# Performance work log

Measured on AMD Instinct MI355X. Metric: run time of the kernel, lower is better.

Reference implementation:

```python
import jax, jax.numpy as jnp
import numpy as np

NA = 100000
NB = 100000
N_REL = 6
REL_SRC = ['A', 'B', 'A', 'B', 'A', 'B']
REL_DST = ['B', 'A', 'A', 'B', 'B', 'A']
N_NODES = {'A': NA, 'B': NB}
H_DIM, OUT_DIM, N_BASES, N_EDGES = 64, 16, 4, 500000


def setup_inputs() -> dict:
    key = jax.random.key(0)
    ks = jax.random.split(key, 16)
    inp = {
        'embed_A': jax.random.normal(ks[0], (NA, H_DIM), jnp.float32) * 0.1,
        'embed_B': jax.random.normal(ks[1], (NB, H_DIM), jnp.float32) * 0.1,
        'bias0': jnp.zeros((H_DIM,), jnp.float32),
        'w_comp1': jax.random.normal(ks[2], (N_REL, N_BASES), jnp.float32) * 0.5,
        'basis1': jax.random.normal(ks[3], (N_BASES, H_DIM, H_DIM), jnp.float32) * (1.0 / np.sqrt(H_DIM)),
        'bias1': jnp.zeros((H_DIM,), jnp.float32),
        'w_comp2': jax.random.normal(ks[4], (N_REL, N_BASES), jnp.float32) * 0.5,
        'basis2': jax.random.normal(ks[5], (N_BASES, H_DIM, OUT_DIM), jnp.float32) * (1.0 / np.sqrt(H_DIM)),
        'bias2': jnp.zeros((OUT_DIM,), jnp.float32),
    }
    for r in range(N_REL):
        inp[f'src_r{r}'] = jax.random.randint(ks[6 + r], (N_EDGES,), 0, N_NODES[REL_SRC[r]], jnp.int32)
        inp[f'dst_r{r}'] = jax.random.randint(jax.random.fold_in(ks[6 + r], 7), (N_EDGES,), 0, N_NODES[REL_DST[r]], jnp.int32)
    return inp


def _hetero_conv(h, W_rels, bias, edges, out_dim, activation):
    # h: dict ntype -> [N, d_in]; W_rels: None or [n_rel, d_in, d_out]
    out = {nt: jnp.zeros((N_NODES[nt], out_dim), h['A'].dtype) for nt in N_NODES}
    for r in range(N_REL):
        src_t, dst_t = REL_SRC[r], REL_DST[r]
        src, dst = edges[r]
        x = h[src_t] if W_rels is None else h[src_t] @ W_rels[r]  # [N_src, d_out]
        msg = x[src]  # gather: [E, d_out]
        n_dst = N_NODES[dst_t]
        agg = jax.ops.segment_sum(msg, dst, num_segments=n_dst)
        deg = jax.ops.segment_sum(jnp.ones((msg.shape[0],), msg.dtype), dst, num_segments=n_dst)
        out[dst_t] = out[dst_t] + agg / jnp.maximum(deg, 1.0)[:, None]  # norm='right'
    out = {nt: out[nt] + bias for nt in out}
    if activation is not None:
        out = {nt: activation(out[nt]) for nt in out}
    return out


def reference(embed_A, embed_B, bias0, w_comp1, basis1, bias1, w_comp2, basis2, bias2,
              src_r0, dst_r0, src_r1, dst_r1, src_r2, dst_r2,
              src_r3, dst_r3, src_r4, dst_r4, src_r5, dst_r5):
    edges = [(src_r0, dst_r0), (src_r1, dst_r1), (src_r2, dst_r2),
             (src_r3, dst_r3), (src_r4, dst_r4), (src_r5, dst_r5)]
    h = {'A': embed_A, 'B': embed_B}
    # layer 0: weight=False -> pure normalized aggregation + bias + relu
    h = _hetero_conv(h, None, bias0, edges, H_DIM, jax.nn.relu)
    # hidden layer with basis-decomposed weights
    W1 = jnp.einsum('rb,bio->rio', w_comp1, basis1)
    h = _hetero_conv(h, W1, bias1, edges, H_DIM, jax.nn.relu)
    # output layer, no activation
    W2 = jnp.einsum('rb,bio->rio', w_comp2, basis2)
    h = _hetero_conv(h, W2, bias2, edges, OUT_DIM, None)
    return h['A']  # logits for category node type
```

## Files before the change

### kernel.cpp

```cpp
#include <hip/hip_runtime.h>

#define NN 100000
#define EE 500000
#define DD 64
#define OD 16
#define NR 6
#define NBASE 4
#define BSH 10
#define NBK 98
#define SBLK 128
#define FLATN (NBK * SBLK)
#define STCAP 5632

struct Edges { const int* src[NR]; const int* dst[NR]; };

typedef __attribute__((ext_vector_type(8))) short bf16x8;
typedef __attribute__((ext_vector_type(4))) float f32x4;

__device__ __forceinline__ float bf2f(ushort u) {
    union { unsigned int i; float f; } v; v.i = ((unsigned int)u) << 16; return v.f;
}
__device__ __forceinline__ ushort f2bf(float f) {
    unsigned int x = __float_as_uint(f);
    unsigned int r = (x + 0x7fffu + ((x >> 16) & 1u)) >> 16;
    return (ushort)r;
}
__device__ __forceinline__ void bfpair(unsigned int u, float& lo, float& hi) {
    lo = __uint_as_float(u << 16);
    hi = __uint_as_float(u & 0xffff0000u);
}

__global__ __launch_bounds__(256) void build_w_kernel(
    const float* __restrict__ wc1, const float* __restrict__ b1,
    const float* __restrict__ wc2, const float* __restrict__ b2,
    ushort* __restrict__ Wp1, ushort* __restrict__ Wp2)
{
    int idx = blockIdx.x * blockDim.x + threadIdx.x;
    const int n1 = NR * DD * DD;
    const int n2 = NR * DD * OD;
    if (idx < n1) {
        int r = idx >> 12, rem = idx & 4095;
        int i = rem >> 6, o = rem & 63;
        float s = 0.f;
        #pragma unroll
        for (int b = 0; b < NBASE; ++b) s += wc1[r * NBASE + b] * b1[b * 4096 + rem];
        Wp1[(((size_t)(r * 8 + (i >> 3)) * 64 + o) << 3) + (i & 7)] = f2bf(s);
    } else if (idx < n1 + n2) {
        int j = idx - n1;
        int r = j >> 10, rem = j & 1023;
        int i = rem >> 4, o = rem & 15;
        float s = 0.f;
        #pragma unroll
        for (int b = 0; b < NBASE; ++b) s += wc2[r * NBASE + b] * b2[b * 1024 + rem];
        Wp2[(((size_t)(r * 8 + (i >> 3)) * 16 + o) << 3) + (i & 7)] = f2bf(s);
    }
}

__global__ __launch_bounds__(256) void cvt_kernel(
    const float* __restrict__ in, ushort* __restrict__ out, int n4)
{
    int i = blockIdx.x * 256 + threadIdx.x;
    if (i >= n4) return;
    float4 v = ((const float4*)in)[i];
    ushort4 o;
    o.x = f2bf(v.x); o.y = f2bf(v.y); o.z = f2bf(v.z); o.w = f2bf(v.w);
    ((ushort4*)out)[i] = o;
}

__global__ __launch_bounds__(256) void count_kernel(Edges ep, int* __restrict__ cnt_mat)
{
    __shared__ int h[NBK];
    int r = blockIdx.y, blk = blockIdx.x;
    const int* __restrict__ dst = ep.dst[r];
    const int chunk = (EE + SBLK - 1) / SBLK;
    int e0 = blk * chunk, e1 = min(e0 + chunk, EE);
    for (int i = threadIdx.x; i < NBK; i += 256) h[i] = 0;
    __syncthreads();
    for (int e = e0 + threadIdx.x; e < e1; e += 256)
        atomicAdd(&h[dst[e] >> BSH], 1);
    __syncthreads();
    for (int b = threadIdx.x; b < NBK; b += 256)
        cnt_mat[r * FLATN + b * SBLK + blk] = h[b];
}

__global__ __launch_bounds__(1024) void flat_scan_kernel(
    const int* __restrict__ cnt_mat, int* __restrict__ off_flat, int* __restrict__ bbase)
{
    __shared__ int wsum[16];
    const int TPE = 13;
    int r = blockIdx.x;
    int tid = threadIdx.x, lane = tid & 63, wid = tid >> 6;
    int base = tid * TPE;
    int v[TPE];
    int s = 0;
    #pragma unroll
    for (int j = 0; j < TPE; ++j) {
        int i = base + j;
        v[j] = (i < FLATN) ? cnt_mat[r * FLATN + i] : 0;
        s += v[j];
    }
    int si = s;
    #pragma unroll
    for (int off = 1; off < 64; off <<= 1) {
        int t = __shfl_up(si, off);
        if (lane >= off) si += t;
    }
    if (lane == 63) wsum[wid] = si;
    __syncthreads();
    if (wid == 0) {
        int ws = (lane < 16) ? wsum[lane] : 0;
        #pragma unroll
        for (int off = 1; off < 16; off <<= 1) {
            int t = __shfl_up(ws, off);
            if (lane >= off) ws += t;
        }
        if (lane < 16) wsum[lane] = ws;
    }
    __syncthreads();
    int texcl = (wid > 0 ? wsum[wid - 1] : 0) + (si - s);
    int part = 0;
    #pragma unroll
    for (int j = 0; j < TPE; ++j) {
        int i = base + j;
        if (i < FLATN) {
            int o = texcl + part;
            off_flat[r * FLATN + i] = o;
            if ((i & (SBLK - 1)) == 0) bbase[r * (NBK + 1) + (i >> 7)] = o;
        }
        part += v[j];
    }
    if (tid == 0) bbase[r * (NBK + 1) + NBK] = EE;
}

__global__ __launch_bounds__(256) void scatter2_kernel(
    Edges ep, const int* __restrict__ off_flat, unsigned int* __restrict__ ebuf)
{
    __shared__ int goff[NBK];
    __shared__ int lcnt[NBK];
    int r = blockIdx.y, blk = blockIdx.x;
    const int* __restrict__ src = ep.src[r];
    const int* __restrict__ dst = ep.dst[r];
    unsigned int* eb = ebuf + (size_t)r * EE;
    const int chunk = (EE + SBLK - 1) / SBLK;
    int e0 = blk * chunk, e1 = min(e0 + chunk, EE);
    if (threadIdx.x < NBK) {
        goff[threadIdx.x] = off_flat[r * FLATN + threadIdx.x * SBLK + blk];
        lcnt[threadIdx.x] = 0;
    }
    __syncthreads();
    for (int e = e0 + threadIdx.x; e < e1; e += 256) {
        int d = dst[e];
        int b = d >> BSH;
        int pos = goff[b] + atomicAdd(&lcnt[b], 1);
        eb[pos] = (unsigned int)src[e] | ((unsigned int)(d & 1023) << 17);
    }
}

__global__ __launch_bounds__(256) void csr_fine_kernel(
    const unsigned int* __restrict__ ebuf, const int* __restrict__ bbase,
    int* __restrict__ row_ptr, float* __restrict__ inv_deg, int* __restrict__ col_idx)
{
    __shared__ int nh[1024];
    __shared__ int nb[1024];
    __shared__ int wsum4[4];
    __shared__ int stage[STCAP];
    int r = blockIdx.y, b = blockIdx.x;
    int tid = threadIdx.x, lane = tid & 63, wid = tid >> 6;
    int gb = bbase[r * (NBK + 1) + b];
    int ge = bbase[r * (NBK + 1) + b + 1];
    int cnt = ge - gb;
    if (cnt > STCAP) cnt = STCAP;
    const unsigned int* eb = ebuf + (size_t)r * EE + gb;
    #pragma unroll
    for (int j = 0; j < 4; ++j) nh[tid * 4 + j] = 0;
    __syncthreads();
    for (int i = tid; i < cnt; i += 256)
        atomicAdd(&nh[(eb[i] >> 17) & 1023], 1);
    __syncthreads();
    int v0 = nh[tid * 4 + 0], v1 = nh[tid * 4 + 1], v2 = nh[tid * 4 + 2], v3 = nh[tid * 4 + 3];
    int s = v0 + v1 + v2 + v3;
    int si = s;
    #pragma unroll
    for (int off = 1; off < 64; off <<= 1) {
        int t = __shfl_up(si, off);
        if (lane >= off) si += t;
    }
    if (lane == 63) wsum4[wid] = si;
    __syncthreads();
    if (tid == 0) {
        int a = 0;
        #pragma unroll
        for (int k = 0; k < 4; ++k) { int t = wsum4[k]; wsum4[k] = a; a += t; }
    }
    __syncthreads();
    int texcl = wsum4[wid] + (si - s);
    int p0 = texcl, p1 = p0 + v0, p2 = p1 + v1, p3 = p2 + v2;
    nb[tid * 4 + 0] = p0; nb[tid * 4 + 1] = p1; nb[tid * 4 + 2] = p2; nb[tid * 4 + 3] = p3;
    {
        int node0 = b * 1024 + tid * 4;
        int pj[4] = { p0, p1, p2, p3 };
        int vj[4] = { v0, v1, v2, v3 };
        #pragma unroll
        for (int j = 0; j < 4; ++j) {
            int node = node0 + j;
            if (node < NN) {
                row_ptr[r * (NN + 1) + node] = gb + pj[j];
                inv_deg[r * NN + node] = 1.0f / (float)(vj[j] > 1 ? vj[j] : 1);
            }
        }
    }
    if (b == NBK - 1 && tid == 0) row_ptr[r * (NN + 1) + NN] = EE;
    #pragma unroll
    for (int j = 0; j < 4; ++j) nh[tid * 4 + j] = 0;
    __syncthreads();
    for (int i = tid; i < cnt; i += 256) {
        unsigned int w = eb[i];
        int loc = (w >> 17) & 1023;
        int pos = nb[loc] + atomicAdd(&nh[loc], 1);
        stage[pos] = (int)(w & 0x1ffffu);
    }
    __syncthreads();
    int* co = col_idx + (size_t)r * EE + gb;
    for (int i = tid; i < cnt; i += 256) co[i] = stage[i];
}

__global__ __launch_bounds__(256) void agg_kernel(
    const ushort* __restrict__ f0, const ushort* __restrict__ f1, const ushort* __restrict__ f2,
    int r0, int r1, int r2,
    const int* __restrict__ row_ptr, const int* __restrict__ col_idx,
    const float* __restrict__ inv_deg, ushort* __restrict__ z)
{
    int tid = threadIdx.x;
    int wid = tid >> 6, lane = tid & 63;
    int grp = lane >> 3;
    int sub = lane & 7;
    int n = blockIdx.x * 32 + wid * 8 + grp;
    int ks = blockIdx.y;
    const ushort* F = (ks == 0) ? f0 : ((ks == 1) ? f1 : f2);
    int r = (ks == 0) ? r0 : ((ks == 1) ? r1 : r2);
    const int* rp = row_ptr + r * (NN + 1);
    const int* ci = col_idx + (size_t)r * EE;
    bool valid = (n < NN);
    int s = valid ? rp[n] : 0;
    int e = valid ? rp[n + 1] : 0;
    float a0 = 0.f, a1 = 0.f, a2 = 0.f, a3 = 0.f, a4 = 0.f, a5 = 0.f, a6 = 0.f, a7 = 0.f;
    for (int t = s; t < e; ++t) {
        int c = ci[t];
        int4 v = *(const int4*)(F + (size_t)c * DD + sub * 8);
        float l0, h0, l1, h1, l2, h2, l3, h3;
        bfpair((unsigned int)v.x, l0, h0);
        bfpair((unsigned int)v.y, l1, h1);
        bfpair((unsigned int)v.z, l2, h2);
        bfpair((unsigned int)v.w, l3, h3);
        a0 += l0; a1 += h0; a2 += l1; a3 += h1;
        a4 += l2; a5 += h2; a6 += l3; a7 += h3;
    }
    if (valid) {
        float inv = inv_deg[r * NN + n];
        int4 o;
        o.x = (int)((unsigned int)f2bf(a0 * inv) | ((unsigned int)f2bf(a1 * inv) << 16));
        o.y = (int)((unsigned int)f2bf(a2 * inv) | ((unsigned int)f2bf(a3 * inv) << 16));
        o.z = (int)((unsigned int)f2bf(a4 * inv) | ((unsigned int)f2bf(a5 * inv) << 16));
        o.w = (int)((unsigned int)f2bf(a6 * inv) | ((unsigned int)f2bf(a7 * inv) << 16));
        *(int4*)(z + (size_t)n * 192 + ks * 64 + sub * 8) = o;
    }
}

__global__ __launch_bounds__(256) void layer0_kernel(
    const ushort* __restrict__ f0, const ushort* __restrict__ f1, const ushort* __restrict__ f2,
    int r0, int r1, int r2,
    const int* __restrict__ row_ptr, const int* __restrict__ col_idx,
    const float* __restrict__ inv_deg, const float* __restrict__ bias,
    ushort* __restrict__ h)
{
    int tid = threadIdx.x;
    int wid = tid >> 6, lane = tid & 63;
    int grp = lane >> 3;
    int sub = lane & 7;
    int n = blockIdx.x * 32 + wid * 8 + grp;
    bool valid = (n < NN);
    float acc[8];
    {
        float4 b0 = *(const float4*)(bias + sub * 8);
        float4 b1 = *(const float4*)(bias + sub * 8 + 4);
        acc[0] = b0.x; acc[1] = b0.y; acc[2] = b0.z; acc[3] = b0.w;
        acc[4] = b1.x; acc[5] = b1.y; acc[6] = b1.z; acc[7] = b1.w;
    }
    #pragma unroll
    for (int ks = 0; ks < 3; ++ks) {
        const ushort* F = (ks == 0) ? f0 : ((ks == 1) ? f1 : f2);
        int r = (ks == 0) ? r0 : ((ks == 1) ? r1 : r2);
        const int* rp = row_ptr + r * (NN + 1);
        const int* ci = col_idx + (size_t)r * EE;
        int s = valid ? rp[n] : 0;
        int e = valid ? rp[n + 1] : 0;
        float a0 = 0.f, a1 = 0.f, a2 = 0.f, a3 = 0.f, a4 = 0.f, a5 = 0.f, a6 = 0.f, a7 = 0.f;
        for (int t = s; t < e; ++t) {
            int c = ci[t];
            int4 v = *(const int4*)(F + (size_t)c * DD + sub * 8);
            float l0, h0, l1, h1, l2, h2, l3, h3;
            bfpair((unsigned int)v.x, l0, h0);
            bfpair((unsigned int)v.y, l1, h1);
            bfpair((unsigned int)v.z, l2, h2);
            bfpair((unsigned int)v.w, l3, h3);
            a0 += l0; a1 += h0; a2 += l1; a3 += h1;
            a4 += l2; a5 += h2; a6 += l3; a7 += h3;
        }
        float inv = valid ? inv_deg[r * NN + n] : 0.f;
        acc[0] += a0 * inv; acc[1] += a1 * inv; acc[2] += a2 * inv; acc[3] += a3 * inv;
        acc[4] += a4 * inv; acc[5] += a5 * inv; acc[6] += a6 * inv; acc[7] += a7 * inv;
    }
    if (valid) {
        int4 o;
        o.x = (int)((unsigned int)f2bf(fmaxf(acc[0], 0.f)) | ((unsigned int)f2bf(fmaxf(acc[1], 0.f)) << 16));
        o.y = (int)((unsigned int)f2bf(fmaxf(acc[2], 0.f)) | ((unsigned int)f2bf(fmaxf(acc[3], 0.f)) << 16));
        o.z = (int)((unsigned int)f2bf(fmaxf(acc[4], 0.f)) | ((unsigned int)f2bf(fmaxf(acc[5], 0.f)) << 16));
        o.w = (int)((unsigned int)f2bf(fmaxf(acc[6], 0.f)) | ((unsigned int)f2bf(fmaxf(acc[7], 0.f)) << 16));
        *(int4*)(h + (size_t)n * DD + sub * 8) = o;
    }
}

__global__ __launch_bounds__(256) void gemm1_mfma_kernel(
    const ushort* __restrict__ A, const ushort* __restrict__ Wp,
    int r0, int r1, int r2, const float* __restrict__ bias, ushort* __restrict__ out)
{
    int tid = threadIdx.x;
    int wave = tid >> 6, lane = tid & 63;
    int q = lane & 15, p = lane >> 4;
    int n0 = blockIdx.x * 64 + wave * 16;
    int rr[3] = { r0, r1, r2 };
    f32x4 acc0 = {0.f, 0.f, 0.f, 0.f};
    f32x4 acc1 = {0.f, 0.f, 0.f, 0.f};
    f32x4 acc2 = {0.f, 0.f, 0.f, 0.f};
    f32x4 acc3 = {0.f, 0.f, 0.f, 0.f};
    const ushort* arow = A + (size_t)(n0 + q) * 192 + p * 8;
    #pragma unroll
    for (int ks = 0; ks < 3; ++ks) {
        int rel = rr[ks];
        #pragma unroll
        for (int t = 0; t < 2; ++t) {
            bf16x8 a = *(const bf16x8*)(arow + ks * 64 + t * 32);
            const ushort* wb = Wp + (((size_t)(rel * 8 + t * 4 + p) * 64 + q) << 3);
            bf16x8 b0 = *(const bf16x8*)(wb);
            bf16x8 b1 = *(const bf16x8*)(wb + 16 * 8);
            bf16x8 b2 = *(const bf16x8*)(wb + 32 * 8);
            bf16x8 b3 = *(const bf16x8*)(wb + 48 * 8);
            acc0 = __builtin_amdgcn_mfma_f32_16x16x32_bf16(a, b0, acc0, 0, 0, 0);
            acc1 = __builtin_amdgcn_mfma_f32_16x16x32_bf16(a, b1, acc1, 0, 0, 0);
            acc2 = __builtin_amdgcn_mfma_f32_16x16x32_bf16(a, b2, acc2, 0, 0, 0);
            acc3 = __builtin_amdgcn_mfma_f32_16x16x32_bf16(a, b3, acc3, 0, 0, 0);
        }
    }
    float bv0 = bias[q], bv1 = bias[16 + q], bv2 = bias[32 + q], bv3 = bias[48 + q];
    #pragma unroll
    for (int v = 0; v < 4; ++v) {
        int n = n0 + p * 4 + v;
        if (n < NN) {
            ushort* orow = out + (size_t)n * 64;
            orow[q]      = f2bf(fmaxf(acc0[v] + bv0, 0.f));
            orow[16 + q] = f2bf(fmaxf(acc1[v] + bv1, 0.f));
            orow[32 + q] = f2bf(fmaxf(acc2[v] + bv2, 0.f));
            orow[48 + q] = f2bf(fmaxf(acc3[v] + bv3, 0.f));
        }
    }
}

__global__ __launch_bounds__(256) void gemm2_mfma_kernel(
    const ushort* __restrict__ A, const ushort* __restrict__ Wp,
    int r0, int r1, int r2, const float* __restrict__ bias, float* __restrict__ out)
{
    int tid = threadIdx.x;
    int wave = tid >> 6, lane = tid & 63;
    int q = lane & 15, p = lane >> 4;
    int n0 = blockIdx.x * 64 + wave * 16;
    int rr[3] = { r0, r1, r2 };
    f32x4 acc = {0.f, 0.f, 0.f, 0.f};
    const ushort* arow = A + (size_t)(n0 + q) * 192 + p * 8;
    #pragma unroll
    for (int ks = 0; ks < 3; ++ks) {
        int rel = rr[ks];
        #pragma unroll
        for (int t = 0; t < 2; ++t) {
            bf16x8 a = *(const bf16x8*)(arow + ks * 64 + t * 32);
            bf16x8 b = *(const bf16x8*)(Wp + (((size_t)(rel * 8 + t * 4 + p) * 16 + q) << 3));
            acc = __builtin_amdgcn_mfma_f32_16x16x32_bf16(a, b, acc, 0, 0, 0);
        }
    }
    float bv = bias[q];
    #pragma unroll
    for (int v = 0; v < 4; ++v) {
        int n = n0 + p * 4 + v;
        if (n < NN) out[(size_t)n * 16 + q] = acc[v] + bv;
    }
}

extern "C" void kernel_launch(void* const* d_in, const int* in_sizes, int n_in,
                              void* d_out, int out_size, void* d_ws, size_t ws_size,
                              hipStream_t stream)
{
    const float* embA  = (const float*)d_in[0];
    const float* embB  = (const float*)d_in[1];
    const float* bias0 = (const float*)d_in[2];
    const float* wc1   = (const float*)d_in[3];
    const float* b1    = (const float*)d_in[4];
    const float* bias1 = (const float*)d_in[5];
    const float* wc2   = (const float*)d_in[6];
    const float* b2    = (const float*)d_in[7];
    const float* bias2 = (const float*)d_in[8];

    Edges ep;
    for (int r = 0; r < NR; ++r) {
        ep.src[r] = (const int*)d_in[9 + 2 * r];
        ep.dst[r] = (const int*)d_in[10 + 2 * r];
    }

    char* ws = (char*)d_ws;
    size_t off = 0;
    auto alloc = [&](size_t bytes) {
        void* p = ws + off;
        off = (off + bytes + 255) & ~(size_t)255;
        return p;
    };
    ushort* Wp1     = (ushort*)alloc((size_t)NR * 8 * 64 * 8 * 2);
    ushort* Wp2     = (ushort*)alloc((size_t)NR * 8 * 16 * 8 * 2);
    int*    cnt_mat = (int*)   alloc((size_t)NR * FLATN * 4);
    int*    off_fl  = (int*)   alloc((size_t)NR * FLATN * 4);
    int*    bbase   = (int*)   alloc((size_t)NR * (NBK + 1) * 4);
    int*    row_ptr = (int*)   alloc((size_t)NR * (NN + 1) * 4);
    float*  inv_deg = (float*) alloc((size_t)NR * NN * 4);
    int*    col_idx = (int*)   alloc((size_t)NR * EE * 4);
    ushort* zA      = (ushort*)alloc((size_t)NN * 192 * 2);
    ushort* zB      = (ushort*)alloc((size_t)NN * 192 * 2);
    ushort* h0A     = (ushort*)alloc((size_t)NN * DD * 2);
    ushort* h0B     = (ushort*)alloc((size_t)NN * DD * 2);
    ushort* h1A     = (ushort*)alloc((size_t)NN * DD * 2);
    ushort* h1B     = (ushort*)alloc((size_t)NN * DD * 2);
    (void)ws_size;

    unsigned int* ebuf   = (unsigned int*)zA;
    ushort*       embA16 = h1A;
    ushort*       embB16 = h1B;

    int nw = NR * DD * DD + NR * DD * OD;
    build_w_kernel<<<(nw + 255) / 256, 256, 0, stream>>>(wc1, b1, wc2, b2, Wp1, Wp2);
    cvt_kernel<<<(NN * DD / 4 + 255) / 256, 256, 0, stream>>>(embA, embA16, NN * DD / 4);
    cvt_kernel<<<(NN * DD / 4 + 255) / 256, 256, 0, stream>>>(embB, embB16, NN * DD / 4);

    count_kernel<<<dim3(SBLK, NR), 256, 0, stream>>>(ep, cnt_mat);
    flat_scan_kernel<<<NR, 1024, 0, stream>>>(cnt_mat, off_fl, bbase);
    scatter2_kernel<<<dim3(SBLK, NR), 256, 0, stream>>>(ep, off_fl, ebuf);
    csr_fine_kernel<<<dim3(NBK, NR), 256, 0, stream>>>(ebuf, bbase, row_ptr, inv_deg, col_idx);

    dim3 agrid((NN + 31) / 32, 3);
    dim3 l0grid((NN + 31) / 32, 1);
    int ggrid = (NN + 63) / 64;

    layer0_kernel<<<l0grid, 256, 0, stream>>>(embB16, embA16, embB16, 1, 2, 5,
                                              row_ptr, col_idx, inv_deg, bias0, h0A);
    layer0_kernel<<<l0grid, 256, 0, stream>>>(embA16, embB16, embA16, 0, 3, 4,
                                              row_ptr, col_idx, inv_deg, bias0, h0B);

    agg_kernel<<<agrid, 256, 0, stream>>>(h0B, h0A, h0B, 1, 2, 5,
                                          row_ptr, col_idx, inv_deg, zA);
    agg_kernel<<<agrid, 256, 0, stream>>>(h0A, h0B, h0A, 0, 3, 4,
                                          row_ptr, col_idx, inv_deg, zB);
    gemm1_mfma_kernel<<<ggrid, 256, 0, stream>>>(zA, Wp1, 1, 2, 5, bias1, h1A);
    gemm1_mfma_kernel<<<ggrid, 256, 0, stream>>>(zB, Wp1, 0, 3, 4, bias1, h1B);

    agg_kernel<<<agrid, 256, 0, stream>>>(h1B, h1A, h1B, 1, 2, 5,
                                          row_ptr, col_idx, inv_deg, zA);
    gemm2_mfma_kernel<<<ggrid, 256, 0, stream>>>(zA, Wp2, 1, 2, 5, bias2, (float*)d_out);
}
```

Baseline: 333.2 us.

## Degree-sort destination nodes for load balance and merge aggregation launches

Builds a per-relation (and per-combined-relation) permutation of destination nodes sorted by degree bucket using a histogram, scan and scatter pass. The aggregation and layer-0 kernels then process nodes in that order, so lanes in a wave see similar edge counts and spend less time idle. The edge loop is also unrolled by two to keep more gathers in flight, and the separate A/B launches are merged into one grid per stage. This adds three preprocessing kernels and an extra indirection, and output writes become scattered rather than contiguous.

```diff
diff --git a/kernel.cpp b/kernel.cpp
--- a/kernel.cpp
+++ b/kernel.cpp
@@ -11,6 +11,10 @@
 #define SBLK 128
 #define FLATN (NBK * SBLK)
 #define STCAP 5632
+#define DBIN 64
+#define DBLK 128
+#define FLAT2 (DBIN * DBLK)
+#define NVR 8
 
 struct Edges { const int* src[NR]; const int* dst[NR]; };
 
@@ -224,36 +228,139 @@
     for (int i = tid; i < cnt; i += 256) co[i] = stage[i];
 }
 
+__device__ __forceinline__ int vdeg(int vr, int n, const int* __restrict__ rp)
+{
+    if (vr < 6) return rp[vr * (NN + 1) + n + 1] - rp[vr * (NN + 1) + n];
+    if (vr == 6)
+        return (rp[1 * (NN + 1) + n + 1] - rp[1 * (NN + 1) + n])
+             + (rp[2 * (NN + 1) + n + 1] - rp[2 * (NN + 1) + n])
+             + (rp[5 * (NN + 1) + n + 1] - rp[5 * (NN + 1) + n]);
+    return (rp[0 * (NN + 1) + n + 1] - rp[0 * (NN + 1) + n])
+         + (rp[3 * (NN + 1) + n + 1] - rp[3 * (NN + 1) + n])
+         + (rp[4 * (NN + 1) + n + 1] - rp[4 * (NN + 1) + n]);
+}
+
+__global__ __launch_bounds__(256) void dhist_kernel(
+    const int* __restrict__ row_ptr, int* __restrict__ cnt2)
+{
+    __shared__ int h[DBIN];
+    int vr = blockIdx.y, blk = blockIdx.x;
+    if (threadIdx.x < DBIN) h[threadIdx.x] = 0;
+    __syncthreads();
+    const int chunk = (NN + DBLK - 1) / DBLK;
+    int n0 = blk * chunk, n1 = min(n0 + chunk, NN);
+    for (int n = n0 + threadIdx.x; n < n1; n += 256)
+        atomicAdd(&h[min(vdeg(vr, n, row_ptr), DBIN - 1)], 1);
+    __syncthreads();
+    if (threadIdx.x < DBIN) cnt2[vr * FLAT2 + threadIdx.x * DBLK + blk] = h[threadIdx.x];
+}
+
+__global__ __launch_bounds__(1024) void dscan_kernel(
+    const int* __restrict__ cnt2, int* __restrict__ off2)
+{
+    __shared__ int wsum[16];
+    const int TPE = 8;
+    int vr = blockIdx.x;
+    int tid = threadIdx.x, lane = tid & 63, wid = tid >> 6;
+    int base = tid * TPE;
+    int v[TPE];
+    int s = 0;
+    #pragma unroll
+    for (int j = 0; j < TPE; ++j) { v[j] = cnt2[vr * FLAT2 + base + j]; s += v[j]; }
+    int si = s;
+    #pragma unroll
+    for (int off = 1; off < 64; off <<= 1) {
+        int t = __shfl_up(si, off);
+        if (lane >= off) si += t;
+    }
+    if (lane == 63) wsum[wid] = si;
+    __syncthreads();
+    if (wid == 0) {
+        int ws = (lane < 16) ? wsum[lane] : 0;
+        #pragma unroll
+        for (int off = 1; off < 16; off <<= 1) {
+            int t = __shfl_up(ws, off);
+            if (lane >= off) ws += t;
+        }
+        if (lane < 16) wsum[lane] = ws;
+    }
+    __syncthreads();
+    int texcl = (wid > 0 ? wsum[wid - 1] : 0) + (si - s);
+    int part = 0;
+    #pragma unroll
+    for (int j = 0; j < TPE; ++j) {
+        off2[vr * FLAT2 + base + j] = texcl + part;
+        part += v[j];
+    }
+}
+
+__global__ __launch_bounds__(256) void dscatter_kernel(
+    const int* __restrict__ row_ptr, const int* __restrict__ off2, int* __restrict__ perm)
+{
+    __shared__ int goff[DBIN];
+    __shared__ int lcnt[DBIN];
+    int vr = blockIdx.y, blk = blockIdx.x;
+    if (threadIdx.x < DBIN) {
+        goff[threadIdx.x] = off2[vr * FLAT2 + threadIdx.x * DBLK + blk];
+        lcnt[threadIdx.x] = 0;
+    }
+    __syncthreads();
+    const int chunk = (NN + DBLK - 1) / DBLK;
+    int n0 = blk * chunk, n1 = min(n0 + chunk, NN);
+    for (int n = n0 + threadIdx.x; n < n1; n += 256) {
+        int b = min(vdeg(vr, n, row_ptr), DBIN - 1);
+        int pos = goff[b] + atomicAdd(&lcnt[b], 1);
+        perm[vr * NN + pos] = n;
+    }
+}
+
 __global__ __launch_bounds__(256) void agg_kernel(
-    const ushort* __restrict__ f0, const ushort* __restrict__ f1, const ushort* __restrict__ f2,
-    int r0, int r1, int r2,
+    const ushort* __restrict__ hA, const ushort* __restrict__ hB,
     const int* __restrict__ row_ptr, const int* __restrict__ col_idx,
-    const float* __restrict__ inv_deg, ushort* __restrict__ z)
-{
+    const float* __restrict__ inv_deg, const int* __restrict__ perm,
+    ushort* __restrict__ zA, ushort* __restrict__ zB)
+{
+    const int relT[6]   = {1, 2, 5, 0, 3, 4};
+    const int srcIsA[6] = {0, 1, 0, 1, 0, 1};
+    int y = blockIdx.y;
+    int r = relT[y];
+    const ushort* F = srcIsA[y] ? hA : hB;
+    ushort* z = (y < 3) ? zA : zB;
+    int ks = (y < 3) ? y : y - 3;
     int tid = threadIdx.x;
     int wid = tid >> 6, lane = tid & 63;
-    int grp = lane >> 3;
-    int sub = lane & 7;
-    int n = blockIdx.x * 32 + wid * 8 + grp;
-    int ks = blockIdx.y;
-    const ushort* F = (ks == 0) ? f0 : ((ks == 1) ? f1 : f2);
-    int r = (ks == 0) ? r0 : ((ks == 1) ? r1 : r2);
+    int grp = lane >> 3, sub = lane & 7;
+    int idx = blockIdx.x * 32 + wid * 8 + grp;
+    bool valid = (idx < NN);
+    int n = valid ? perm[r * NN + idx] : 0;
     const int* rp = row_ptr + r * (NN + 1);
     const int* ci = col_idx + (size_t)r * EE;
-    bool valid = (n < NN);
     int s = valid ? rp[n] : 0;
     int e = valid ? rp[n + 1] : 0;
     float a0 = 0.f, a1 = 0.f, a2 = 0.f, a3 = 0.f, a4 = 0.f, a5 = 0.f, a6 = 0.f, a7 = 0.f;
-    for (int t = s; t < e; ++t) {
-        int c = ci[t];
-        int4 v = *(const int4*)(F + (size_t)c * DD + sub * 8);
-        float l0, h0, l1, h1, l2, h2, l3, h3;
-        bfpair((unsigned int)v.x, l0, h0);
-        bfpair((unsigned int)v.y, l1, h1);
-        bfpair((unsigned int)v.z, l2, h2);
-        bfpair((unsigned int)v.w, l3, h3);
-        a0 += l0; a1 += h0; a2 += l1; a3 += h1;
-        a4 += l2; a5 += h2; a6 += l3; a7 += h3;
+    int t = s;
+    for (; t + 2 <= e; t += 2) {
+        int c0 = ci[t], c1 = ci[t + 1];
+        int4 u = *(const int4*)(F + (size_t)c0 * DD + sub * 8);
+        int4 w = *(const int4*)(F + (size_t)c1 * DD + sub * 8);
+        float l, h;
+        bfpair((unsigned int)u.x, l, h); a0 += l; a1 += h;
+        bfpair((unsigned int)u.y, l, h); a2 += l; a3 += h;
+        bfpair((unsigned int)u.z, l, h); a4 += l; a5 += h;
+        bfpair((unsigned int)u.w, l, h); a6 += l; a7 += h;
+        bfpair((unsigned int)w.x, l, h); a0 += l; a1 += h;
+        bfpair((unsigned int)w.y, l, h); a2 += l; a3 += h;
+        bfpair((unsigned int)w.z, l, h); a4 += l; a5 += h;
+        bfpair((unsigned int)w.w, l, h); a6 += l; a7 += h;
+    }
+    if (t < e) {
+        int c0 = ci[t];
+        int4 u = *(const int4*)(F + (size_t)c0 * DD + sub * 8);
+        float l, h;
+        bfpair((unsigned int)u.x, l, h); a0 += l; a1 += h;
+        bfpair((unsigned int)u.y, l, h); a2 += l; a3 += h;
+        bfpair((unsigned int)u.z, l, h); a4 += l; a5 += h;
+        bfpair((unsigned int)u.w, l, h); a6 += l; a7 += h;
     }
     if (valid) {
         float inv = inv_deg[r * NN + n];
@@ -267,18 +374,19 @@
 }
 
 __global__ __launch_bounds__(256) void layer0_kernel(
-    const ushort* __restrict__ f0, const ushort* __restrict__ f1, const ushort* __restrict__ f2,
-    int r0, int r1, int r2,
+    const ushort* __restrict__ eA, const ushort* __restrict__ eB,
     const int* __restrict__ row_ptr, const int* __restrict__ col_idx,
-    const float* __restrict__ inv_deg, const float* __restrict__ bias,
-    ushort* __restrict__ h)
-{
+    const float* __restrict__ inv_deg, const int* __restrict__ perm,
+    const float* __restrict__ bias, ushort* __restrict__ hA, ushort* __restrict__ hB)
+{
+    int side = blockIdx.y;
+    const int relT[2][3] = { {1, 2, 5}, {0, 3, 4} };
     int tid = threadIdx.x;
     int wid = tid >> 6, lane = tid & 63;
-    int grp = lane >> 3;
-    int sub = lane & 7;
-    int n = blockIdx.x * 32 + wid * 8 + grp;
-    bool valid = (n < NN);
+    int grp = lane >> 3, sub = lane & 7;
+    int idx = blockIdx.x * 32 + wid * 8 + grp;
+    bool valid = (idx < NN);
+    int n = valid ? perm[(6 + side) * NN + idx] : 0;
     float acc[8];
     {
         float4 b0 = *(const float4*)(bias + sub * 8);
@@ -288,29 +396,43 @@
     }
     #pragma unroll
     for (int ks = 0; ks < 3; ++ks) {
-        const ushort* F = (ks == 0) ? f0 : ((ks == 1) ? f1 : f2);
-        int r = (ks == 0) ? r0 : ((ks == 1) ? r1 : r2);
+        int r = relT[side][ks];
+        const ushort* F = ((side == 0) == (ks == 1)) ? eA : eB;
         const int* rp = row_ptr + r * (NN + 1);
         const int* ci = col_idx + (size_t)r * EE;
         int s = valid ? rp[n] : 0;
         int e = valid ? rp[n + 1] : 0;
         float a0 = 0.f, a1 = 0.f, a2 = 0.f, a3 = 0.f, a4 = 0.f, a5 = 0.f, a6 = 0.f, a7 = 0.f;
-        for (int t = s; t < e; ++t) {
-            int c = ci[t];
-            int4 v = *(const int4*)(F + (size_t)c * DD + sub * 8);
-            float l0, h0, l1, h1, l2, h2, l3, h3;
-            bfpair((unsigned int)v.x, l0, h0);
-            bfpair((unsigned int)v.y, l1, h1);
-            bfpair((unsigned int)v.z, l2, h2);
-            bfpair((unsigned int)v.w, l3, h3);
-            a0 += l0; a1 += h0; a2 += l1; a3 += h1;
-            a4 += l2; a5 += h2; a6 += l3; a7 += h3;
+        int t = s;
+        for (; t + 2 <= e; t += 2) {
+            int c0 = ci[t], c1 = ci[t + 1];
+            int4 u = *(const int4*)(F + (size_t)c0 * DD + sub * 8);
+            int4 w = *(const int4*)(F + (size_t)c1 * DD + sub * 8);
+            float l, h;
+            bfpair((unsigned int)u.x, l, h); a0 += l; a1 += h;
+            bfpair((unsigned int)u.y, l, h); a2 += l; a3 += h;
+            bfpair((unsigned int)u.z, l, h); a4 += l; a5 += h;
+            bfpair((unsigned int)u.w, l, h); a6 += l; a7 += h;
+            bfpair((unsigned int)w.x, l, h); a0 += l; a1 += h;
+            bfpair((unsigned int)w.y, l, h); a2 += l; a3 += h;
+            bfpair((unsigned int)w.z, l, h); a4 += l; a5 += h;
+            bfpair((unsigned int)w.w, l, h); a6 += l; a7 += h;
+        }
+        if (t < e) {
+            int c0 = ci[t];
+            int4 u = *(const int4*)(F + (size_t)c0 * DD + sub * 8);
+            float l, h;
+            bfpair((unsigned int)u.x, l, h); a0 += l; a1 += h;
+            bfpair((unsigned int)u.y, l, h); a2 += l; a3 += h;
+            bfpair((unsigned int)u.z, l, h); a4 += l; a5 += h;
+            bfpair((unsigned int)u.w, l, h); a6 += l; a7 += h;
         }
         float inv = valid ? inv_deg[r * NN + n] : 0.f;
         acc[0] += a0 * inv; acc[1] += a1 * inv; acc[2] += a2 * inv; acc[3] += a3 * inv;
         acc[4] += a4 * inv; acc[5] += a5 * inv; acc[6] += a6 * inv; acc[7] += a7 * inv;
     }
     if (valid) {
+        ushort* h = side ? hB : hA;
         int4 o;
         o.x = (int)((unsigned int)f2bf(fmaxf(acc[0], 0.f)) | ((unsigned int)f2bf(fmaxf(acc[1], 0.f)) << 16));
         o.y = (int)((unsigned int)f2bf(fmaxf(acc[2], 0.f)) | ((unsigned int)f2bf(fmaxf(acc[3], 0.f)) << 16));
@@ -429,6 +551,7 @@
     int*    row_ptr = (int*)   alloc((size_t)NR * (NN + 1) * 4);
     float*  inv_deg = (float*) alloc((size_t)NR * NN * 4);
     int*    col_idx = (int*)   alloc((size_t)NR * EE * 4);
+    int*    perm    = (int*)   alloc((size_t)NVR * NN * 4);
     ushort* zA      = (ushort*)alloc((size_t)NN * 192 * 2);
     ushort* zB      = (ushort*)alloc((size_t)NN * 192 * 2);
     ushort* h0A     = (ushort*)alloc((size_t)NN * DD * 2);
@@ -440,6 +563,8 @@
     unsigned int* ebuf   = (unsigned int*)zA;
     ushort*       embA16 = h1A;
     ushort*       embB16 = h1B;
+    int*          cnt2   = cnt_mat;
+    int*          off2   = off_fl;
 
     int nw = NR * DD * DD + NR * DD * OD;
     build_w_kernel<<<(nw + 255) / 256, 256, 0, stream>>>(wc1, b1, wc2, b2, Wp1, Wp2);
@@ -451,23 +576,22 @@
     scatter2_kernel<<<dim3(SBLK, NR), 256, 0, stream>>>(ep, off_fl, ebuf);
     csr_fine_kernel<<<dim3(NBK, NR), 256, 0, stream>>>(ebuf, bbase, row_ptr, inv_deg, col_idx);
 
-    dim3 agrid((NN + 31) / 32, 3);
-    dim3 l0grid((NN + 31) / 32, 1);
+    dhist_kernel<<<dim3(DBLK, NVR), 256, 0, stream>>>(row_ptr, cnt2);
+    dscan_kernel<<<NVR, 1024, 0, stream>>>(cnt2, off2);
+    dscatter_kernel<<<dim3(DBLK, NVR), 256, 0, stream>>>(row_ptr, off2, perm);
+
+    int agx = (NN + 31) / 32;
     int ggrid = (NN + 63) / 64;
 
-    layer0_kernel<<<l0grid, 256, 0, stream>>>(embB16, embA16, embB16, 1, 2, 5,
-                                              row_ptr, col_idx, inv_deg, bias0, h0A);
-    layer0_kernel<<<l0grid, 256, 0, stream>>>(embA16, embB16, embA16, 0, 3, 4,
-                                              row_ptr, col_idx, inv_deg, bias0, h0B);
-
-    agg_kernel<<<agrid, 256, 0, stream>>>(h0B, h0A, h0B, 1, 2, 5,
-                                          row_ptr, col_idx, inv_deg, zA);
-    agg_kernel<<<agrid, 256, 0, stream>>>(h0A, h0B, h0A, 0, 3, 4,
-                                          row_ptr, col_idx, inv_deg, zB);
+    layer0_kernel<<<dim3(agx, 2), 256, 0, stream>>>(
+        embA16, embB16, row_ptr, col_idx, inv_deg, perm, bias0, h0A, h0B);
+
+    agg_kernel<<<dim3(agx, 6), 256, 0, stream>>>(
+        h0A, h0B, row_ptr, col_idx, inv_deg, perm, zA, zB);
     gemm1_mfma_kernel<<<ggrid, 256, 0, stream>>>(zA, Wp1, 1, 2, 5, bias1, h1A);
     gemm1_mfma_kernel<<<ggrid, 256, 0, stream>>>(zB, Wp1, 0, 3, 4, bias1, h1B);
 
-    agg_kernel<<<agrid, 256, 0, stream>>>(h1B, h1A, h1B, 1, 2, 5,
-                                          row_ptr, col_idx, inv_deg, zA);
+    agg_kernel<<<dim3(agx, 3), 256, 0, stream>>>(
+        h1A, h1B, row_ptr, col_idx, inv_deg, perm, zA, zB);
     gemm2_mfma_kernel<<<ggrid, 256, 0, stream>>>(zA, Wp2, 1, 2, 5, bias2, (float*)d_out);
 }
```

Result: faster. 310.7 us (-6.7%).
